# Kernel tuning notes

Measured on AMD Instinct MI355X. Metric: run time of the kernel, lower is better.

The kernel has to match this reference:

```python
import jax, jax.numpy as jnp
import numpy as np

B, S, D, H = 2, 2048, 1024, 16
HD = D // H  # 64
SCALE = float(np.sqrt(HD))


def setup_inputs() -> dict:
    key = jax.random.key(0)
    ks = jax.random.split(key, 5)
    x = jax.random.normal(ks[0], (B, S, D), dtype=jnp.float32)
    # causal mask: 1 = attend, 0 = masked
    mask = jnp.tril(jnp.ones((S, S), dtype=jnp.int32))
    xavier = lambda k: jax.random.normal(k, (D, D), dtype=jnp.float32) * np.sqrt(2.0 / (D + D))
    return {
        "x": x,
        "mask": mask,
        "Wq": xavier(ks[1]),
        "Wk": xavier(ks[2]),
        "Wv": xavier(ks[3]),
        "Wo": xavier(ks[4]),
    }


def reference(x, mask, Wq, Wk, Wv, Wo):
    # torch Linear(bias=False): y = x @ W.T  with W of shape [out, in]
    def heads(W):
        return (x @ W.T).reshape(B, S, H, HD).transpose(0, 2, 1, 3)  # [B,H,S,HD]

    Q, K, V = heads(Wq), heads(Wk), heads(Wv)
    scores = jnp.einsum("bhqd,bhkd->bhqk", Q, K) / SCALE  # [B,H,S,S]
    scores = jnp.where(mask[None, None] == 0, -jnp.inf, scores)
    attn = jax.nn.softmax(scores, axis=-1)
    attn = jnp.where(jnp.isnan(attn), jnp.zeros_like(attn), attn)  # nan-fix for fully masked rows
    # dropout is identity in eval / p=0
    out = jnp.einsum("bhqk,bhkd->bhqd", attn, V)  # [B,H,S,HD]
    out = out.transpose(0, 2, 1, 3).reshape(B, S, D)
    return out @ Wo.T
```

## Files before the change

kernel.cpp:

```cpp
#include <hip/hip_runtime.h>


using bfx8 = __attribute__((ext_vector_type(8))) short;
using fx4  = __attribute__((ext_vector_type(4))) float;

#define NB 2
#define NS 2048
#define ND 1024
#define NH 16
#define NHD 64

__device__ __forceinline__ unsigned short f2bf(float f) {
  union { float f; unsigned u; } v; v.f = f;
  return (unsigned short)((v.u + 0x7fffu + ((v.u >> 16) & 1u)) >> 16);
}
__device__ __forceinline__ unsigned pk2(float a, float b) {
  return (unsigned)f2bf(a) | ((unsigned)f2bf(b) << 16);
}
__device__ __forceinline__ unsigned pkt(float a, float b) {
  union { float f; unsigned u; } ua, ub; ua.f = a; ub.f = b;
  return (ua.u >> 16) | (ub.u & 0xffff0000u);
}
__device__ __forceinline__ int vperm32(int k5) {
  return (((k5 & 15) >> 2) << 3) + (((k5 >> 4) & 1) << 2) + (k5 & 3);
}

#define GLD16(gp, lp) __builtin_amdgcn_global_load_lds( \
    (__attribute__((address_space(1))) void*)(gp),      \
    (__attribute__((address_space(3))) void*)(lp), 16, 0, 0)

__global__ __launch_bounds__(256)
void cvt_all(const float4* __restrict__ x,  const float4* __restrict__ wq,
             const float4* __restrict__ wk, const float4* __restrict__ wv,
             const float4* __restrict__ wo, unsigned short* __restrict__ dst) {
  const int NT4 = (NB * NS * ND) / 4, NW4 = (ND * ND) / 4;
  const int i = blockIdx.x * 256 + threadIdx.x;
  const float4* src;
  int off;
  if (i < NT4) {
    src = x; off = i;
  } else {
    const int k = i - NT4;
    const int seg = k / NW4;
    off = k - seg * NW4;
    src = (seg == 0) ? wq : (seg == 1) ? wk : (seg == 2) ? wv : wo;
  }
  float4 f = src[off];
  uint2 w;
  w.x = pk2(f.x, f.y);
  w.y = pk2(f.z, f.w);
  *(uint2*)(dst + (size_t)i * 4) = w;
}

__global__ __launch_bounds__(256)
void gemm_qkvT(const unsigned short* __restrict__ Wcat,
               const unsigned short* __restrict__ xb,
               unsigned short* __restrict__ Qb, unsigned short* __restrict__ Kb,
               unsigned short* __restrict__ Vt, float SCL) {
  __shared__ __attribute__((aligned(16))) unsigned short As[3][128 * 32];
  __shared__ __attribute__((aligned(16))) unsigned short Bs[3][128 * 32];
  const int t = threadIdx.x;
  const int lane = t & 63, wave = t >> 6;
  const int wr = wave >> 1, wc = wave & 1;
  const int r16 = lane & 15, quad = lane >> 4;
  const int n0 = blockIdx.x * 128;
  const int m0 = blockIdx.y * 128;
  const int KD = 1024;
  fx4 acc[4][4] = {};
  const int c0 = t, c1 = t + 256;
  const size_t a0 = (size_t)(n0 + (c0 >> 2)) * KD + (size_t)(((c0 & 3) ^ ((c0 >> 3) & 3)) * 8);
  const size_t a1 = (size_t)(n0 + (c1 >> 2)) * KD + (size_t)(((c1 & 3) ^ ((c1 >> 3) & 3)) * 8);
  const size_t b0 = (size_t)(m0 + (c0 >> 2)) * KD + (size_t)(((c0 & 3) ^ ((c0 >> 3) & 3)) * 8);
  const size_t b1 = (size_t)(m0 + (c1 >> 2)) * KD + (size_t)(((c1 & 3) ^ ((c1 >> 3) & 3)) * 8);

#define QKVT_STAGE(bi, kk) do {                      \
    GLD16(Wcat + a0 + (kk), &As[bi][c0 * 8]);        \
    GLD16(Wcat + a1 + (kk), &As[bi][c1 * 8]);        \
    GLD16(xb   + b0 + (kk), &Bs[bi][c0 * 8]);        \
    GLD16(xb   + b1 + (kk), &Bs[bi][c1 * 8]);        \
  } while (0)

  QKVT_STAGE(0, 0);
  QKVT_STAGE(1, 32);
  QKVT_STAGE(2, 64);
  const int swr = (quad ^ ((r16 >> 1) & 3)) * 8;
  int cur = 0;
  for (int k0 = 0; k0 < KD; k0 += 32) {
    asm volatile("s_waitcnt vmcnt(8)" ::: "memory");
    __builtin_amdgcn_s_barrier();
    bfx8 af[4], bfr[4];
#pragma unroll
    for (int ni = 0; ni < 4; ni++)
      af[ni] = *(const bfx8*)&As[cur][(wr * 64 + ni * 16 + r16) * 32 + swr];
#pragma unroll
    for (int mi = 0; mi < 4; mi++)
      bfr[mi] = *(const bfx8*)&Bs[cur][(wc * 64 + mi * 16 + r16) * 32 + swr];
#pragma unroll
    for (int ni = 0; ni < 4; ni++)
#pragma unroll
      for (int mi = 0; mi < 4; mi++)
        acc[ni][mi] = __builtin_amdgcn_mfma_f32_16x16x32_bf16(
            af[ni], bfr[mi], acc[ni][mi], 0, 0, 0);
    __builtin_amdgcn_s_barrier();
    int kn = k0 + 96;
    if (kn >= KD) kn = KD - 32;
    QKVT_STAGE(cur, kn);
    cur = (cur == 2) ? 0 : cur + 1;
  }
#undef QKVT_STAGE
#pragma unroll
  for (int ni = 0; ni < 4; ni++) {
#pragma unroll
    for (int mi = 0; mi < 4; mi++) {
      fx4 v = acc[ni][mi];
      const int n = n0 + wr * 64 + ni * 16 + quad * 4;
      const int m = m0 + wc * 64 + mi * 16 + r16;
      const int b = m >> 11, s = m & (NS - 1);
      if (n0 < 1024) {
        const int h = n >> 6, hd = n & (NHD - 1);
        const size_t base = ((size_t)(b * NH + h) * NS + s) * NHD + hd;
        uint2 pw;
        pw.x = pk2(v[0] * SCL, v[1] * SCL);
        pw.y = pk2(v[2] * SCL, v[3] * SCL);
        *(uint2*)(Qb + base) = pw;
      } else if (n0 < 2048) {
        const int n2 = n - 1024;
        const int h = n2 >> 6, hd = n2 & (NHD - 1);
        const size_t base = ((size_t)(b * NH + h) * NS + s) * NHD + hd;
        uint2 pw;
        pw.x = pk2(v[0], v[1]);
        pw.y = pk2(v[2], v[3]);
        *(uint2*)(Kb + base) = pw;
      } else {
        const int n2 = n - 2048;
        const int h = n2 >> 6, hd = n2 & (NHD - 1);
        const int sp = (s & ~31) | vperm32(s & 31);
        const size_t base = ((size_t)(b * NH + h) * NHD + hd) * NS + sp;
#pragma unroll
        for (int r = 0; r < 4; r++) Vt[base + (size_t)r * NS] = f2bf(v[r]);
      }
    }
  }
}

__global__ __launch_bounds__(256)
void gemm_qkv_f32(const float* __restrict__ x,
                  const float* __restrict__ W0, const float* __restrict__ W1,
                  const float* __restrict__ W2,
                  unsigned short* __restrict__ Qb, unsigned short* __restrict__ Kb,
                  unsigned short* __restrict__ Vt, float SCL) {
  __shared__ __attribute__((aligned(16))) unsigned short As[128 * 32];
  __shared__ __attribute__((aligned(16))) unsigned short Bs[128 * 32];
  const int t = threadIdx.x;
  const int lane = t & 63, wave = t >> 6;
  const int wr = wave >> 1, wc = wave & 1;
  const int r16 = lane & 15, quad = lane >> 4;
  const int m0 = blockIdx.x * 128, n0 = blockIdx.y * 128;
  const int z = blockIdx.z;
  const float* W = (z == 0) ? W0 : (z == 1) ? W1 : W2;
  const int KD = 1024;
  fx4 acc[4][4] = {};
  const int row2 = t >> 1, kh = t & 1;
  for (int k0 = 0; k0 < KD; k0 += 32) {
    {
      const float4* src = (const float4*)(x + (size_t)(m0 + row2) * KD + k0 + kh * 16);
      float4 f0 = src[0], f1 = src[1], f2 = src[2], f3 = src[3];
      uint4 w0 = {pk2(f0.x, f0.y), pk2(f0.z, f0.w), pk2(f1.x, f1.y), pk2(f1.z, f1.w)};
      uint4 w1 = {pk2(f2.x, f2.y), pk2(f2.z, f2.w), pk2(f3.x, f3.y), pk2(f3.z, f3.w)};
      *(uint4*)&As[row2 * 32 + kh * 16] = w0;
      *(uint4*)&As[row2 * 32 + kh * 16 + 8] = w1;
    }
    {
      const float4* src = (const float4*)(W + (size_t)(n0 + row2) * KD + k0 + kh * 16);
      float4 f0 = src[0], f1 = src[1], f2 = src[2], f3 = src[3];
      uint4 w0 = {pk2(f0.x, f0.y), pk2(f0.z, f0.w), pk2(f1.x, f1.y), pk2(f1.z, f1.w)};
      uint4 w1 = {pk2(f2.x, f2.y), pk2(f2.z, f2.w), pk2(f3.x, f3.y), pk2(f3.z, f3.w)};
      *(uint4*)&Bs[row2 * 32 + kh * 16] = w0;
      *(uint4*)&Bs[row2 * 32 + kh * 16 + 8] = w1;
    }
    __syncthreads();
    bfx8 af[4], bfr[4];
#pragma unroll
    for (int mt = 0; mt < 4; mt++)
      af[mt] = *(const bfx8*)&As[(wr * 64 + mt * 16 + r16) * 32 + quad * 8];
#pragma unroll
    for (int nt = 0; nt < 4; nt++)
      bfr[nt] = *(const bfx8*)&Bs[(wc * 64 + nt * 16 + r16) * 32 + quad * 8];
#pragma unroll
    for (int mt = 0; mt < 4; mt++)
#pragma unroll
      for (int nt = 0; nt < 4; nt++)
        acc[mt][nt] = __builtin_amdgcn_mfma_f32_16x16x32_bf16(
            af[mt], bfr[nt], acc[mt][nt], 0, 0, 0);
    __syncthreads();
  }
#pragma unroll
  for (int mt = 0; mt < 4; mt++) {
#pragma unroll
    for (int nt = 0; nt < 4; nt++) {
      fx4 v = acc[mt][nt];
      const int mb = m0 + wr * 64 + mt * 16 + quad * 4;
      const int n = n0 + wc * 64 + nt * 16 + r16;
      const int b = mb >> 11, s = mb & (NS - 1);
      const int h = n >> 6, hd = n & (NHD - 1);
      if (z <= 1) {
        unsigned short* C = (z == 0) ? Qb : Kb;
        const float sc = (z == 0) ? SCL : 1.0f;
        const size_t base = ((size_t)(b * NH + h) * NS + s) * NHD + hd;
#pragma unroll
        for (int r = 0; r < 4; r++) C[base + (size_t)r * NHD] = f2bf(v[r] * sc);
      } else {
        const int sp = (s & ~31) | (((s & 15) >> 2) << 3) | (((s >> 4) & 1) << 2);
        const size_t base = ((size_t)(b * NH + h) * NHD + hd) * NS + sp;
        uint2 pw;
        pw.x = pk2(v[0], v[1]);
        pw.y = pk2(v[2], v[3]);
        *(uint2*)(Vt + base) = pw;
      }
    }
  }
}

template <bool BF16>
__global__ __launch_bounds__(256)
void gemm_out(const unsigned short* __restrict__ A,
              const void* __restrict__ Wv,
              float* __restrict__ C) {
  __shared__ __attribute__((aligned(16))) unsigned short As[64 * 64];
  __shared__ __attribute__((aligned(16))) unsigned short Bs[128 * 64];
  const int t = threadIdx.x;
  const int lane = t & 63, wave = t >> 6;
  const int wr = wave >> 1, wc = wave & 1;
  const int r16 = lane & 15, quad = lane >> 4;
  const int m0 = blockIdx.x * 64, n0 = blockIdx.y * 128;
  const int KD = 1024;
  fx4 acc[2][4] = {};
  for (int k0 = 0; k0 < KD; k0 += 64) {
#pragma unroll
    for (int cc = 0; cc < 2; cc++) {
      const int c = t + cc * 256;
      GLD16(A + (size_t)(m0 + (c >> 3)) * KD + (size_t)(((c & 7) ^ ((c >> 3) & 7)) * 8) + k0,
            &As[c * 8]);
    }
    if constexpr (BF16) {
      const unsigned short* W = (const unsigned short*)Wv;
#pragma unroll
      for (int cc = 0; cc < 4; cc++) {
        const int c = t + cc * 256;
        GLD16(W + (size_t)(n0 + (c >> 3)) * KD + (size_t)(((c & 7) ^ ((c >> 3) & 7)) * 8) + k0,
              &Bs[c * 8]);
      }
    } else {
      const float* W = (const float*)Wv;
#pragma unroll
      for (int cc = 0; cc < 4; cc++) {
        const int c = t + cc * 256;
        const float4* src = (const float4*)(W + (size_t)(n0 + (c >> 3)) * KD +
                                            ((c & 7) ^ ((c >> 3) & 7)) * 8 + k0);
        float4 f0 = src[0], f1 = src[1];
        uint4 w0 = {pk2(f0.x, f0.y), pk2(f0.z, f0.w), pk2(f1.x, f1.y), pk2(f1.z, f1.w)};
        *(uint4*)&Bs[c * 8] = w0;
      }
    }
    __syncthreads();
    bfx8 af[2][2], bfr[4][2];
#pragma unroll
    for (int ks = 0; ks < 2; ks++) {
      const int sw = ((ks * 4 + quad) ^ (r16 & 7)) * 8;
#pragma unroll
      for (int mt = 0; mt < 2; mt++)
        af[mt][ks] = *(const bfx8*)&As[(wr * 32 + mt * 16 + r16) * 64 + sw];
#pragma unroll
      for (int nt = 0; nt < 4; nt++)
        bfr[nt][ks] = *(const bfx8*)&Bs[(wc * 64 + nt * 16 + r16) * 64 + sw];
    }
#pragma unroll
    for (int ks = 0; ks < 2; ks++)
#pragma unroll
      for (int mt = 0; mt < 2; mt++)
#pragma unroll
        for (int nt = 0; nt < 4; nt++)
          acc[mt][nt] = __builtin_amdgcn_mfma_f32_16x16x32_bf16(
              af[mt][ks], bfr[nt][ks], acc[mt][nt], 0, 0, 0);
    __syncthreads();
  }
#pragma unroll
  for (int mt = 0; mt < 2; mt++) {
#pragma unroll
    for (int nt = 0; nt < 4; nt++) {
      fx4 v = acc[mt][nt];
      const int s = m0 + wr * 32 + mt * 16 + quad * 4;
      const int n = n0 + wc * 64 + nt * 16 + r16;
      const size_t base = (size_t)s * ND + n;
#pragma unroll
      for (int r = 0; r < 4; r++) C[base + (size_t)r * ND] = v[r];
    }
  }
}

__global__ __launch_bounds__(512)
void attn_mfma(const unsigned short* __restrict__ Q,
               const unsigned short* __restrict__ K,
               const unsigned short* __restrict__ Vt,
               unsigned short* __restrict__ O) {
  __shared__ __attribute__((aligned(16))) unsigned short Ks[64 * 64];
  __shared__ __attribute__((aligned(16))) unsigned short Vs[64 * 64];
  const int t = threadIdx.x;
  const int lane = t & 63, wave = t >> 6;
  const int r16 = lane & 15, quad = lane >> 4;
  const int bh = blockIdx.x;
  const int by = blockIdx.y;
  const int tile = (by < 8) ? (15 - by) : (by - 8);
  const int b = bh >> 4, h = bh & (NH - 1);
  const int q0b = tile * 128;
  const int qbase = q0b + r16 * 8 + wave;
  const int nT = 2 * tile + 2;
  const unsigned short* Qp = Q + (size_t)bh * NS * NHD;
  const unsigned short* Kp = K + (size_t)bh * NS * NHD;
  const unsigned short* Vp = Vt + (size_t)bh * NHD * NS;

  bfx8 qf[2];
#pragma unroll
  for (int hs = 0; hs < 2; hs++)
    qf[hs] = *(const bfx8*)&Qp[(size_t)qbase * NHD + hs * 32 + quad * 8];

  fx4 acc[4] = {};
  float lsum = 0.0f;

  const int c0 = t;
  const int ls0 = (c0 >> 3) * 64 + (((c0 & 7) ^ ((c0 >> 3) & 7)) * 8);
  const int rx = r16 & 7;
  uint4 kr0 = *(const uint4*)&Kp[8 * c0];
  uint4 vr0 = *(const uint4*)&Vp[(size_t)(c0 >> 3) * NS + (c0 & 7) * 8];

  for (int tt = 0; tt < nT; tt++) {
    __syncthreads();
    *(uint4*)&Ks[ls0] = kr0;
    *(uint4*)&Vs[ls0] = vr0;
    if (tt + 1 < nT) {
      const int kk = (tt + 1) * 64;
      kr0 = *(const uint4*)&Kp[kk * 64 + 8 * c0];
      vr0 = *(const uint4*)&Vp[(size_t)(c0 >> 3) * NS + kk + (c0 & 7) * 8];
    }
    __syncthreads();

#pragma unroll
    for (int ks32 = 0; ks32 < 2; ks32++) {
      const int kkeff = tt * 64 + ks32 * 32;
      bfx8 kf[2][2];
      bfx8 vf[4];
#pragma unroll
      for (int kt = 0; kt < 2; kt++)
#pragma unroll
        for (int hs = 0; hs < 2; hs++)
          kf[kt][hs] = *(const bfx8*)&Ks[(ks32 * 32 + kt * 16 + r16) * 64 +
                                         (((hs * 4 + quad) ^ rx) * 8)];
#pragma unroll
      for (int mt = 0; mt < 4; mt++)
        vf[mt] = *(const bfx8*)&Vs[(mt * 16 + r16) * 64 +
                                   (((ks32 * 4 + quad) ^ rx) * 8)];

      fx4 st[2] = {};
      __builtin_amdgcn_s_setprio(1);
#pragma unroll
      for (int kt = 0; kt < 2; kt++)
#pragma unroll
        for (int hs = 0; hs < 2; hs++)
          st[kt] = __builtin_amdgcn_mfma_f32_16x16x32_bf16(
              kf[kt][hs], qf[hs], st[kt], 0, 0, 0);
      __builtin_amdgcn_s_setprio(0);

      if (kkeff >= q0b) {
#pragma unroll
        for (int kt = 0; kt < 2; kt++)
#pragma unroll
          for (int r = 0; r < 4; r++) {
            const int key = kkeff + kt * 16 + quad * 4 + r;
            if (key > qbase) st[kt][r] = -1e30f;
          }
      }

      float p[2][4];
      float ps = 0.0f;
#pragma unroll
      for (int kt = 0; kt < 2; kt++)
#pragma unroll
        for (int r = 0; r < 4; r++) {
          p[kt][r] = __builtin_amdgcn_exp2f(st[kt][r]);
          ps += p[kt][r];
        }
      lsum += ps;
      uint4 pbu;
      pbu.x = pkt(p[0][0], p[0][1]);
      pbu.y = pkt(p[0][2], p[0][3]);
      pbu.z = pkt(p[1][0], p[1][1]);
      pbu.w = pkt(p[1][2], p[1][3]);
      bfx8 pb = *(bfx8*)&pbu;
      __builtin_amdgcn_s_setprio(1);
#pragma unroll
      for (int mt = 0; mt < 4; mt++)
        acc[mt] = __builtin_amdgcn_mfma_f32_16x16x32_bf16(
            vf[mt], pb, acc[mt], 0, 0, 0);
      __builtin_amdgcn_s_setprio(0);
    }
  }

  {
    float l = lsum;
    l += __shfl_xor(l, 16);
    l += __shfl_xor(l, 32);
    const float rinv = 1.0f / l;
    const int s = qbase;
#pragma unroll
    for (int mt = 0; mt < 4; mt++) {
      const int d = h * NHD + mt * 16 + quad * 4;
      uint2 pw;
      pw.x = pk2(acc[mt][0] * rinv, acc[mt][1] * rinv);
      pw.y = pk2(acc[mt][2] * rinv, acc[mt][3] * rinv);
      *(uint2*)(O + ((size_t)b * NS + s) * ND + d) = pw;
    }
  }
}

extern "C" void kernel_launch(void* const* d_in, const int* in_sizes, int n_in,
                              void* d_out, int out_size, void* d_ws, size_t ws_size,
                              hipStream_t stream) {
  const float* x  = (const float*)d_in[0];
  const float* Wq = (const float*)d_in[2];
  const float* Wk = (const float*)d_in[3];
  const float* Wv = (const float*)d_in[4];
  const float* Wo = (const float*)d_in[5];
  float* out = (float*)d_out;
  unsigned short* ws = (unsigned short*)d_ws;
  const float QSCL = 0.125f * 1.44269504f;
  dim3 blk(256);
  const size_t NT = (size_t)NB * NS * ND;
  const size_t NW = (size_t)ND * ND;

  if (ws_size >= (size_t)48 * 1024 * 1024) {
    unsigned short* xb   = ws;
    unsigned short* Wcat = ws + NT;
    unsigned short* Wob  = ws + NT + 3 * NW;
    unsigned short* Qb   = ws + NT + 4 * NW;
    unsigned short* Kb   = Qb + NT;
    unsigned short* Vt   = Qb + 2 * NT;
    unsigned short* Ob   = Qb + 3 * NT;
    const int total4 = (int)((NT + 4 * NW) / 4);
    hipLaunchKernelGGL(cvt_all, dim3(total4 / 256), blk, 0, stream,
                       (const float4*)x, (const float4*)Wq, (const float4*)Wk,
                       (const float4*)Wv, (const float4*)Wo, xb);
    hipLaunchKernelGGL(gemm_qkvT, dim3(24, 32), blk, 0, stream,
                       Wcat, xb, Qb, Kb, Vt, QSCL);
    hipLaunchKernelGGL(attn_mfma, dim3(32, 16), dim3(512), 0, stream,
                       Qb, Kb, Vt, Ob);
    hipLaunchKernelGGL((gemm_out<true>), dim3(64, 8), blk, 0, stream, Ob, Wob, out);
  } else if (ws_size >= (size_t)32 * 1024 * 1024) {
    unsigned short* Qb = ws;
    unsigned short* Kb = ws + NT;
    unsigned short* Vt = ws + 2 * NT;
    unsigned short* Ob = ws + 3 * NT;
    hipLaunchKernelGGL(gemm_qkv_f32, dim3(32, 8, 3), blk, 0, stream,
                       x, Wq, Wk, Wv, Qb, Kb, Vt, QSCL);
    hipLaunchKernelGGL(attn_mfma, dim3(32, 16), dim3(512), 0, stream,
                       Qb, Kb, Vt, Ob);
    hipLaunchKernelGGL((gemm_out<false>), dim3(64, 8), blk, 0, stream, Ob, Wo, out);
  } else {
    const size_t NBA = (size_t)NS * ND;
    unsigned short* Qb = ws;
    unsigned short* Kb = ws + NBA;
    unsigned short* Vt = ws + 2 * NBA;
    unsigned short* Ob = ws + 3 * NBA;
    for (int b = 0; b < NB; b++) {
      const float* xb = x + (size_t)b * NS * ND;
      float* ob = out + (size_t)b * NS * ND;
      hipLaunchKernelGGL(gemm_qkv_f32, dim3(16, 8, 3), blk, 0, stream,
                         xb, Wq, Wk, Wv, Qb, Kb, Vt, QSCL);
      hipLaunchKernelGGL(attn_mfma, dim3(16, 16), dim3(512), 0, stream,
                         Qb, Kb, Vt, Ob);
      hipLaunchKernelGGL((gemm_out<false>), dim3(32, 8), blk, 0, stream, Ob, Wo, ob);
    }
  }
}
```

Measured before the change: 174.4 us.

## Triple-buffer output projection GEMM with async global-to-LDS loads

Splits the output projection GEMM into bf16 and f32 variants. The bf16 path now uses a three-stage LDS ring with K-step 32, issuing direct global-to-LDS loads two stages ahead and using vmcnt waits plus raw barriers, so memory latency overlaps with MFMA work. This replaces the single-buffer load, sync, compute loop. In exchange it adds redundant tail loads, clamped to the last tile, and a new swizzle that could cause bank conflicts or correctness problems if the vmcnt count is wrong.

Result: no change. 174.2 us (-0.1%).

```diff
diff --git a/kernel.cpp b/kernel.cpp
--- a/kernel.cpp
+++ b/kernel.cpp
@@ -221,11 +221,76 @@
   }
 }
 
-template <bool BF16>
 __global__ __launch_bounds__(256)
-void gemm_out(const unsigned short* __restrict__ A,
-              const void* __restrict__ Wv,
-              float* __restrict__ C) {
+void gemm_out_bf16(const unsigned short* __restrict__ A,
+                   const unsigned short* __restrict__ W,
+                   float* __restrict__ C) {
+  __shared__ __attribute__((aligned(16))) unsigned short As[3][64 * 32];
+  __shared__ __attribute__((aligned(16))) unsigned short Bs[3][128 * 32];
+  const int t = threadIdx.x;
+  const int lane = t & 63, wave = t >> 6;
+  const int wr = wave >> 1, wc = wave & 1;
+  const int r16 = lane & 15, quad = lane >> 4;
+  const int m0 = blockIdx.x * 64, n0 = blockIdx.y * 128;
+  const int KD = 1024;
+  fx4 acc[2][4] = {};
+  const int c0 = t, c1 = t + 256;
+  const size_t a0 = (size_t)(m0 + (c0 >> 2)) * KD + (size_t)(((c0 & 3) ^ ((c0 >> 3) & 3)) * 8);
+  const size_t b0 = (size_t)(n0 + (c0 >> 2)) * KD + (size_t)(((c0 & 3) ^ ((c0 >> 3) & 3)) * 8);
+  const size_t b1 = (size_t)(n0 + (c1 >> 2)) * KD + (size_t)(((c1 & 3) ^ ((c1 >> 3) & 3)) * 8);
+
+#define GOUT_STAGE(bi, kk) do {                   \
+    GLD16(A + a0 + (kk), &As[bi][c0 * 8]);        \
+    GLD16(W + b0 + (kk), &Bs[bi][c0 * 8]);        \
+    GLD16(W + b1 + (kk), &Bs[bi][c1 * 8]);        \
+  } while (0)
+
+  GOUT_STAGE(0, 0);
+  GOUT_STAGE(1, 32);
+  GOUT_STAGE(2, 64);
+  const int swr = (quad ^ ((r16 >> 1) & 3)) * 8;
+  int cur = 0;
+  for (int k0 = 0; k0 < KD; k0 += 32) {
+    asm volatile("s_waitcnt vmcnt(6)" ::: "memory");
+    __builtin_amdgcn_s_barrier();
+    bfx8 af[2], bfr[4];
+#pragma unroll
+    for (int mt = 0; mt < 2; mt++)
+      af[mt] = *(const bfx8*)&As[cur][(wr * 32 + mt * 16 + r16) * 32 + swr];
+#pragma unroll
+    for (int nt = 0; nt < 4; nt++)
+      bfr[nt] = *(const bfx8*)&Bs[cur][(wc * 64 + nt * 16 + r16) * 32 + swr];
+#pragma unroll
+    for (int mt = 0; mt < 2; mt++)
+#pragma unroll
+      for (int nt = 0; nt < 4; nt++)
+        acc[mt][nt] = __builtin_amdgcn_mfma_f32_16x16x32_bf16(
+            af[mt], bfr[nt], acc[mt][nt], 0, 0, 0);
+    __builtin_amdgcn_s_barrier();
+    int kn = k0 + 96;
+    if (kn >= KD) kn = KD - 32;
+    GOUT_STAGE(cur, kn);
+    cur = (cur == 2) ? 0 : cur + 1;
+  }
+#undef GOUT_STAGE
+#pragma unroll
+  for (int mt = 0; mt < 2; mt++) {
+#pragma unroll
+    for (int nt = 0; nt < 4; nt++) {
+      fx4 v = acc[mt][nt];
+      const int s = m0 + wr * 32 + mt * 16 + quad * 4;
+      const int n = n0 + wc * 64 + nt * 16 + r16;
+      const size_t base = (size_t)s * ND + n;
+#pragma unroll
+      for (int r = 0; r < 4; r++) C[base + (size_t)r * ND] = v[r];
+    }
+  }
+}
+
+__global__ __launch_bounds__(256)
+void gemm_out_f32(const unsigned short* __restrict__ A,
+                  const float* __restrict__ W,
+                  float* __restrict__ C) {
   __shared__ __attribute__((aligned(16))) unsigned short As[64 * 64];
   __shared__ __attribute__((aligned(16))) unsigned short Bs[128 * 64];
   const int t = threadIdx.x;
@@ -242,25 +307,14 @@
       GLD16(A + (size_t)(m0 + (c >> 3)) * KD + (size_t)(((c & 7) ^ ((c >> 3) & 7)) * 8) + k0,
             &As[c * 8]);
     }
-    if constexpr (BF16) {
-      const unsigned short* W = (const unsigned short*)Wv;
-#pragma unroll
-      for (int cc = 0; cc < 4; cc++) {
-        const int c = t + cc * 256;
-        GLD16(W + (size_t)(n0 + (c >> 3)) * KD + (size_t)(((c & 7) ^ ((c >> 3) & 7)) * 8) + k0,
-              &Bs[c * 8]);
-      }
-    } else {
-      const float* W = (const float*)Wv;
-#pragma unroll
-      for (int cc = 0; cc < 4; cc++) {
-        const int c = t + cc * 256;
-        const float4* src = (const float4*)(W + (size_t)(n0 + (c >> 3)) * KD +
-                                            ((c & 7) ^ ((c >> 3) & 7)) * 8 + k0);
-        float4 f0 = src[0], f1 = src[1];
-        uint4 w0 = {pk2(f0.x, f0.y), pk2(f0.z, f0.w), pk2(f1.x, f1.y), pk2(f1.z, f1.w)};
-        *(uint4*)&Bs[c * 8] = w0;
-      }
+#pragma unroll
+    for (int cc = 0; cc < 4; cc++) {
+      const int c = t + cc * 256;
+      const float4* src = (const float4*)(W + (size_t)(n0 + (c >> 3)) * KD +
+                                          ((c & 7) ^ ((c >> 3) & 7)) * 8 + k0);
+      float4 f0 = src[0], f1 = src[1];
+      uint4 w0 = {pk2(f0.x, f0.y), pk2(f0.z, f0.w), pk2(f1.x, f1.y), pk2(f1.z, f1.w)};
+      *(uint4*)&Bs[c * 8] = w0;
     }
     __syncthreads();
     bfx8 af[2][2], bfr[4][2];
@@ -453,7 +507,7 @@
                        Wcat, xb, Qb, Kb, Vt, QSCL);
     hipLaunchKernelGGL(attn_mfma, dim3(32, 16), dim3(512), 0, stream,
                        Qb, Kb, Vt, Ob);
-    hipLaunchKernelGGL((gemm_out<true>), dim3(64, 8), blk, 0, stream, Ob, Wob, out);
+    hipLaunchKernelGGL(gemm_out_bf16, dim3(64, 8), blk, 0, stream, Ob, Wob, out);
   } else if (ws_size >= (size_t)32 * 1024 * 1024) {
     unsigned short* Qb = ws;
     unsigned short* Kb = ws + NT;
@@ -463,7 +517,7 @@
                        x, Wq, Wk, Wv, Qb, Kb, Vt, QSCL);
     hipLaunchKernelGGL(attn_mfma, dim3(32, 16), dim3(512), 0, stream,
                        Qb, Kb, Vt, Ob);
-    hipLaunchKernelGGL((gemm_out<false>), dim3(64, 8), blk, 0, stream, Ob, Wo, out);
+    hipLaunchKernelGGL(gemm_out_f32, dim3(64, 8), blk, 0, stream, Ob, Wo, out);
   } else {
     const size_t NBA = (size_t)NS * ND;
     unsigned short* Qb = ws;
@@ -477,7 +531,7 @@
                          xb, Wq, Wk, Wv, Qb, Kb, Vt, QSCL);
       hipLaunchKernelGGL(attn_mfma, dim3(16, 16), dim3(512), 0, stream,
                          Qb, Kb, Vt, Ob);
-      hipLaunchKernelGGL((gemm_out<false>), dim3(32, 8), blk, 0, stream, Ob, Wo, ob);
-    }
-  }
-}
+      hipLaunchKernelGGL(gemm_out_f32, dim3(32, 8), blk, 0, stream, Ob, Wo, ob);
+    }
+  }
+}
```
